# Kernel tuning notes

Hardware: AMD Instinct MI355X
Metric: run time of the kernel (lower is better)

Reference implementation:

```python
import jax, jax.numpy as jnp
import numpy as np

N_PEGS = 32      # 33 holes, one empty at start
N_ACTIONS = 132  # 33 positions * 4 moves


def _constants():
    # English peg-solitaire board: 7x7 cross, 33 holes; hole 0 is the center (3,3).
    moves = np.array([[-1, 0], [1, 0], [0, -1], [0, 1]], dtype=np.int64)
    cells = [(i, j) for i in range(7) for j in range(7) if (2 <= i <= 4) or (2 <= j <= 4)]
    cells.remove((3, 3))
    grid = np.array([(3, 3)] + cells, dtype=np.int64)          # (33, 2)
    p2i = {tuple(p): k for k, p in enumerate(grid)}
    pos_ids = np.repeat(np.arange(33), 4)                      # (132,)
    move_ids = np.tile(np.arange(4), 33)                       # (132,)
    apos = grid[pos_ids]                                       # (132, 2)
    amov = moves[move_ids]
    midp = apos + amov
    tgtp = apos + 2 * amov
    mid_idx = np.array([p2i.get(tuple(p), 0) for p in midp], dtype=np.int64)
    tgt_idx = np.array([p2i.get(tuple(p), 0) for p in tgtp], dtype=np.int64)
    oob = np.array([(tuple(m) not in p2i) or (tuple(t) not in p2i)
                    for m, t in zip(midp, tgtp)], dtype=bool)  # (132,)
    return dict(
        action_pos_ids=jnp.asarray(pos_ids, dtype=jnp.int32),
        action_mid_indices=jnp.asarray(mid_idx, dtype=jnp.int32),
        action_target_indices=jnp.asarray(tgt_idx, dtype=jnp.int32),
        oob_mask=jnp.asarray(oob),
        i_indices=jnp.asarray(grid[:, 0], dtype=jnp.int32),
        j_indices=jnp.asarray(grid[:, 1], dtype=jnp.int32),
    )


def setup_inputs() -> dict:
    key = jax.random.key(0)
    n = 262144
    k1, k2, k3, k4 = jax.random.split(key, 4)
    pegs = (jax.random.uniform(k1, (n, 33)) > 0.5).astype(jnp.float32)
    n_pegs = jax.random.randint(k2, (n,), 2, 32).astype(jnp.int32)
    done = jnp.zeros((n,), dtype=bool)
    total_reward = jax.random.uniform(k3, (n,), dtype=jnp.float32)
    actions = jax.random.randint(k4, (n,), 0, N_ACTIONS).astype(jnp.int32)
    inp = {"pegs": pegs, "n_pegs": n_pegs, "done": done,
           "total_reward": total_reward, "actions": actions}
    inp.update(_constants())
    return inp


def _feasible(pegs, done, action_pos_ids, action_mid_indices,
              action_target_indices, oob_mask):
    # (n, 132) boolean feasible-action mask
    mask = ~oob_mask[None, :]
    no_peg = pegs == 0.0
    mask = mask & ~no_peg[:, action_pos_ids]          # source must have a peg
    mask = mask & (pegs[:, action_mid_indices] > 0)   # mid must have a peg
    mask = mask & (pegs[:, action_target_indices] == 0)  # target must be empty
    return mask & ~done[:, None]


def reference(pegs, n_pegs, done, total_reward, actions,
              action_pos_ids, action_mid_indices, action_target_indices,
              oob_mask, i_indices, j_indices):
    n = pegs.shape[0]
    env = jnp.arange(n)
    pos = action_pos_ids[actions]
    mid = action_mid_indices[actions]
    tgt = action_target_indices[actions]
    # execute the jump (same write order as torch: pos<-0, mid<-0, target<-1)
    pegs = pegs.at[env, pos].set(0.0).at[env, mid].set(0.0).at[env, tgt].set(1.0)
    n_pegs = n_pegs - 1
    rewards = jnp.where(n_pegs == 1, 1.0, 1.0 / (N_PEGS - 1)).astype(jnp.float32)
    done_win = n_pegs == 1
    feasible = _feasible(pegs, done, action_pos_ids, action_mid_indices,
                         action_target_indices, oob_mask)
    done_new = done_win | ~feasible.any(axis=1)
    total_reward = total_reward + rewards
    # state: (n, 7, 7, 3)
    ch0 = jnp.zeros((n, 7, 7), dtype=pegs.dtype).at[:, i_indices, j_indices].set(pegs)
    npf = n_pegs.astype(jnp.float32)
    peg_ratio = (npf - 1.0) / (N_PEGS - 1)
    removed_ratio = (N_PEGS - npf) / (N_PEGS - 1)
    states = jnp.stack([
        ch0,
        jnp.broadcast_to(peg_ratio[:, None, None], (n, 7, 7)),
        jnp.broadcast_to(removed_ratio[:, None, None], (n, 7, 7)),
    ], axis=-1)
    return rewards, states, done_new, pegs, n_pegs, total_reward
```

## Files before the change

kernel.cpp:

```cpp
#include <hip/hip_runtime.h>


#define EPB 256
#define NTH 256

constexpr unsigned long long cross_mask() {
    unsigned long long b = 0;
    for (int i = 0; i < 7; ++i)
        for (int j = 0; j < 7; ++j)
            if ((i >= 2 && i <= 4) || (j >= 2 && j <= 4))
                b |= 1ull << (i * 7 + j);
    return b;
}
constexpr unsigned long long cols_le(int jmax) {
    unsigned long long b = 0;
    for (int i = 0; i < 7; ++i)
        for (int j = 0; j <= jmax; ++j) b |= 1ull << (i * 7 + j);
    return b;
}
constexpr unsigned long long cols_ge(int jmin) {
    unsigned long long b = 0;
    for (int i = 0; i < 7; ++i)
        for (int j = jmin; j < 7; ++j) b |= 1ull << (i * 7 + j);
    return b;
}
constexpr unsigned long long B_MASK = cross_mask();
constexpr unsigned long long C_LE4  = cols_le(4);
constexpr unsigned long long C_GE2  = cols_ge(2);

__global__ __launch_bounds__(NTH) void peg_step(
    const float* __restrict__ pegs_in,
    const int* __restrict__ n_pegs_in,
    const unsigned char* __restrict__ done_in,
    const float* __restrict__ tot_rew_in,
    const int* __restrict__ actions,
    const int* __restrict__ pos_ids,
    const int* __restrict__ mid_idx,
    const int* __restrict__ tgt_idx,
    const int* __restrict__ i_ind,
    const int* __restrict__ j_ind,
    float* __restrict__ out,
    int n)
{
    __shared__ __align__(16) float s_pegs[EPB * 33];
    __shared__ int s_pos[132], s_mid[132], s_tgt[132];
    __shared__ int s_c2b[33];
    __shared__ unsigned long long s_bb[EPB];
    __shared__ float s_r1[EPB], s_r2[EPB];

    const int t  = threadIdx.x;
    const int e0 = blockIdx.x * EPB;
    const int e  = e0 + t;

    const int a        = actions[e];
    const int np_new   = n_pegs_in[e] - 1;
    const bool done_old = (done_in[e] != 0);
    const float tot    = tot_rew_in[e];

    if (t < 132) { s_pos[t] = pos_ids[t]; s_mid[t] = mid_idx[t]; s_tgt[t] = tgt_idx[t]; }
    if (t < 33)  s_c2b[t] = i_ind[t] * 7 + j_ind[t];

    {
        const float4* src = (const float4*)(pegs_in + (size_t)e0 * 33);
        float4* dst = (float4*)s_pegs;
        #pragma unroll
        for (int i = t; i < EPB * 33 / 4; i += NTH) dst[i] = src[i];
    }
    __syncthreads();

    float* row = s_pegs + t * 33;
    row[s_pos[a]] = 0.0f;
    row[s_mid[a]] = 0.0f;
    row[s_tgt[a]] = 1.0f;

    unsigned long long P = 0;
    #pragma unroll
    for (int c = 0; c < 33; ++c)
        P |= (unsigned long long)(row[c] != 0.0f) << s_c2b[c];

    const unsigned long long E = ~P & B_MASK;
    const unsigned long long feas =
        (P & (P >> 1) & (E >> 2)  & C_LE4) |
        (P & (P << 1) & (E << 2)  & C_GE2) |
        (P & (P >> 7) & (E >> 14))         |
        (P & (P << 7) & (E << 14));

    const float rw  = (np_new == 1) ? 1.0f : (1.0f / 31.0f);
    const bool  dn  = (np_new == 1) | done_old | (feas == 0ull);
    const float npf = (float)np_new;

    out[e]                    = rw;
    out[(size_t)148 * n + e]  = dn ? 1.0f : 0.0f;
    out[(size_t)182 * n + e]  = npf;
    out[(size_t)183 * n + e]  = tot + rw;

    s_bb[t] = P;
    s_r1[t] = (npf - 1.0f)  * (1.0f / 31.0f);
    s_r2[t] = (32.0f - npf) * (1.0f / 31.0f);
    __syncthreads();

    {
        const float4* src = (const float4*)s_pegs;
        float4* dst = (float4*)(out + (size_t)149 * n + (size_t)e0 * 33);
        #pragma unroll
        for (int i = t; i < EPB * 33 / 4; i += NTH) dst[i] = src[i];
    }

    {
        float4* dst = (float4*)(out + (size_t)n + (size_t)e0 * 147);
        const int total = EPB * 147 / 4;
        for (int q = t; q < total; q += NTH) {
            int f4  = q * 4;
            int env = f4 / 147;
            int el  = f4 - env * 147;
            unsigned long long bb = s_bb[env];
            float r1 = s_r1[env], r2 = s_r2[env];
            float v[4];
            #pragma unroll
            for (int r = 0; r < 4; ++r) {
                if (el == 147) {
                    el = 0; ++env;
                    bb = s_bb[env]; r1 = s_r1[env]; r2 = s_r2[env];
                }
                int rc = el / 3;
                int ch = el - rc * 3;
                float x = (ch == 0) ? (float)((unsigned int)(bb >> rc) & 1u)
                                    : ((ch == 1) ? r1 : r2);
                v[r] = x;
                ++el;
            }
            dst[q] = make_float4(v[0], v[1], v[2], v[3]);
        }
    }
}

extern "C" void kernel_launch(void* const* d_in, const int* in_sizes, int n_in,
                              void* d_out, int out_size, void* d_ws, size_t ws_size,
                              hipStream_t stream) {
    const float* pegs          = (const float*)d_in[0];
    const int* n_pegs          = (const int*)d_in[1];
    const unsigned char* done  = (const unsigned char*)d_in[2];
    const float* total_reward  = (const float*)d_in[3];
    const int* actions         = (const int*)d_in[4];
    const int* pos_ids         = (const int*)d_in[5];
    const int* mid_idx         = (const int*)d_in[6];
    const int* tgt_idx         = (const int*)d_in[7];
    const int* i_ind           = (const int*)d_in[9];
    const int* j_ind           = (const int*)d_in[10];
    float* out = (float*)d_out;

    int n = in_sizes[1];
    dim3 grid(n / EPB), block(NTH);
    hipLaunchKernelGGL(peg_step, grid, block, 0, stream,
                       pegs, n_pegs, done, total_reward, actions,
                       pos_ids, mid_idx, tgt_idx, i_ind, j_ind, out, n);
}
```

Before: 45.43 us.

## Use direct global-to-LDS loads, compute action indices inline, nontemporal stores

```diff
diff --git a/kernel.cpp b/kernel.cpp
--- a/kernel.cpp
+++ b/kernel.cpp
@@ -3,6 +3,26 @@
 
 #define EPB 256
 #define NTH 256
+
+typedef float f32x4 __attribute__((ext_vector_type(4)));
+
+__device__ __forceinline__ bool inboard(int i, int j) {
+    return ((unsigned)i < 7u) && ((unsigned)j < 7u) &&
+           (((i >= 2) && (i <= 4)) || ((j >= 2) && (j <= 4)));
+}
+
+__device__ constexpr int C2B[33] = {
+    24,  2,  3,  4,  9, 10, 11, 14, 15, 16, 17, 18, 19, 20,
+    21, 22, 23, 25, 26, 27, 28, 29, 30, 31, 32, 33, 34,
+    37, 38, 39, 44, 45, 46};
+__device__ constexpr unsigned char B2C[49] = {
+    0, 0, 1, 2, 3, 0, 0,
+    0, 0, 4, 5, 6, 0, 0,
+    7, 8, 9,10,11,12,13,
+   14,15,16, 0,17,18,19,
+   20,21,22,23,24,25,26,
+    0, 0,27,28,29, 0, 0,
+    0, 0,30,31,32, 0, 0};
 
 constexpr unsigned long long cross_mask() {
     unsigned long long b = 0;
@@ -34,17 +54,10 @@
     const unsigned char* __restrict__ done_in,
     const float* __restrict__ tot_rew_in,
     const int* __restrict__ actions,
-    const int* __restrict__ pos_ids,
-    const int* __restrict__ mid_idx,
-    const int* __restrict__ tgt_idx,
-    const int* __restrict__ i_ind,
-    const int* __restrict__ j_ind,
     float* __restrict__ out,
     int n)
 {
     __shared__ __align__(16) float s_pegs[EPB * 33];
-    __shared__ int s_pos[132], s_mid[132], s_tgt[132];
-    __shared__ int s_c2b[33];
     __shared__ unsigned long long s_bb[EPB];
     __shared__ float s_r1[EPB], s_r2[EPB];
 
@@ -52,31 +65,52 @@
     const int e0 = blockIdx.x * EPB;
     const int e  = e0 + t;
 
-    const int a        = actions[e];
-    const int np_new   = n_pegs_in[e] - 1;
+    {
+        const char* src = (const char*)(pegs_in + (size_t)e0 * 33);
+        char* dst = (char*)s_pegs;
+        #pragma unroll
+        for (int i = t; i < EPB * 33 / 4; i += NTH) {
+            __builtin_amdgcn_global_load_lds(
+                (const __attribute__((address_space(1))) void*)(src + 16 * (size_t)i),
+                (__attribute__((address_space(3))) void*)(dst + 16 * (size_t)i),
+                16, 0, 0);
+        }
+    }
+
+    const int a         = actions[e];
+    const int np_new    = n_pegs_in[e] - 1;
     const bool done_old = (done_in[e] != 0);
-    const float tot    = tot_rew_in[e];
+    const float tot     = tot_rew_in[e];
 
-    if (t < 132) { s_pos[t] = pos_ids[t]; s_mid[t] = mid_idx[t]; s_tgt[t] = tgt_idx[t]; }
-    if (t < 33)  s_c2b[t] = i_ind[t] * 7 + j_ind[t];
+    const float rw  = (np_new == 1) ? 1.0f : (1.0f / 31.0f);
+    const float npf = (float)np_new;
+    out[e]                   = rw;
+    out[(size_t)182 * n + e] = npf;
+    out[(size_t)183 * n + e] = tot + rw;
 
-    {
-        const float4* src = (const float4*)(pegs_in + (size_t)e0 * 33);
-        float4* dst = (float4*)s_pegs;
-        #pragma unroll
-        for (int i = t; i < EPB * 33 / 4; i += NTH) dst[i] = src[i];
-    }
+    const int p  = a >> 2;
+    const int mv = a & 3;
+    const int pb = C2B[p];
+    const int pi = pb / 7, pj = pb % 7;
+    const int di = (mv == 0) ? -1 : (mv == 1) ? 1 : 0;
+    const int dj = (mv == 2) ? -1 : (mv == 3) ? 1 : 0;
+    const int db = di * 7 + dj;
+    const bool mid_in = inboard(pi + di, pj + dj);
+    const bool tgt_in = inboard(pi + 2 * di, pj + 2 * dj);
+    const int mid_c = mid_in ? (int)B2C[pb + db]     : 0;
+    const int tgt_c = tgt_in ? (int)B2C[pb + 2 * db] : 0;
+
     __syncthreads();
 
     float* row = s_pegs + t * 33;
-    row[s_pos[a]] = 0.0f;
-    row[s_mid[a]] = 0.0f;
-    row[s_tgt[a]] = 1.0f;
+    row[p]     = 0.0f;
+    row[mid_c] = 0.0f;
+    row[tgt_c] = 1.0f;
 
     unsigned long long P = 0;
     #pragma unroll
     for (int c = 0; c < 33; ++c)
-        P |= (unsigned long long)(row[c] != 0.0f) << s_c2b[c];
+        P |= (unsigned long long)(row[c] != 0.0f) << C2B[c];
 
     const unsigned long long E = ~P & B_MASK;
     const unsigned long long feas =
@@ -85,14 +119,8 @@
         (P & (P >> 7) & (E >> 14))         |
         (P & (P << 7) & (E << 14));
 
-    const float rw  = (np_new == 1) ? 1.0f : (1.0f / 31.0f);
-    const bool  dn  = (np_new == 1) | done_old | (feas == 0ull);
-    const float npf = (float)np_new;
-
-    out[e]                    = rw;
-    out[(size_t)148 * n + e]  = dn ? 1.0f : 0.0f;
-    out[(size_t)182 * n + e]  = npf;
-    out[(size_t)183 * n + e]  = tot + rw;
+    const bool dn = (np_new == 1) | done_old | (feas == 0ull);
+    out[(size_t)148 * n + e] = dn ? 1.0f : 0.0f;
 
     s_bb[t] = P;
     s_r1[t] = (npf - 1.0f)  * (1.0f / 31.0f);
@@ -100,14 +128,14 @@
     __syncthreads();
 
     {
-        const float4* src = (const float4*)s_pegs;
-        float4* dst = (float4*)(out + (size_t)149 * n + (size_t)e0 * 33);
-        #pragma unroll
-        for (int i = t; i < EPB * 33 / 4; i += NTH) dst[i] = src[i];
+        const f32x4* src = (const f32x4*)s_pegs;
+        f32x4* dst = (f32x4*)(out + (size_t)149 * n + (size_t)e0 * 33);
+        for (int i = t; i < EPB * 33 / 4; i += NTH)
+            __builtin_nontemporal_store(src[i], dst + i);
     }
 
     {
-        float4* dst = (float4*)(out + (size_t)n + (size_t)e0 * 147);
+        f32x4* dst = (f32x4*)(out + (size_t)n + (size_t)e0 * 147);
         const int total = EPB * 147 / 4;
         for (int q = t; q < total; q += NTH) {
             int f4  = q * 4;
@@ -115,7 +143,7 @@
             int el  = f4 - env * 147;
             unsigned long long bb = s_bb[env];
             float r1 = s_r1[env], r2 = s_r2[env];
-            float v[4];
+            f32x4 v;
             #pragma unroll
             for (int r = 0; r < 4; ++r) {
                 if (el == 147) {
@@ -124,12 +152,11 @@
                 }
                 int rc = el / 3;
                 int ch = el - rc * 3;
-                float x = (ch == 0) ? (float)((unsigned int)(bb >> rc) & 1u)
-                                    : ((ch == 1) ? r1 : r2);
-                v[r] = x;
+                v[r] = (ch == 0) ? (float)((unsigned int)(bb >> rc) & 1u)
+                                 : ((ch == 1) ? r1 : r2);
                 ++el;
             }
-            dst[q] = make_float4(v[0], v[1], v[2], v[3]);
+            __builtin_nontemporal_store(v, dst + q);
         }
     }
 }
@@ -142,16 +169,10 @@
     const unsigned char* done  = (const unsigned char*)d_in[2];
     const float* total_reward  = (const float*)d_in[3];
     const int* actions         = (const int*)d_in[4];
-    const int* pos_ids         = (const int*)d_in[5];
-    const int* mid_idx         = (const int*)d_in[6];
-    const int* tgt_idx         = (const int*)d_in[7];
-    const int* i_ind           = (const int*)d_in[9];
-    const int* j_ind           = (const int*)d_in[10];
     float* out = (float*)d_out;
 
     int n = in_sizes[1];
     dim3 grid(n / EPB), block(NTH);
     hipLaunchKernelGGL(peg_step, grid, block, 0, stream,
-                       pegs, n_pegs, done, total_reward, actions,
-                       pos_ids, mid_idx, tgt_idx, i_ind, j_ind, out, n);
+                       pegs, n_pegs, done, total_reward, actions, out, n);
 }
```

New measurement: 51.04 us. 12.4% more time.
